# Performance work log

Hardware: AMD Instinct MI355X
Metric: run time of the kernel (lower is better)

## Reference

```python
import jax, jax.numpy as jnp
import numpy as np

N = 4096          # number of video frames (n)
M = 1024          # input feature size (m)
D = 1024          # output_size; must equal M for the grid_sample offset math
APPERTURE = 256   # band half-width: logits with |i-j| >= APPERTURE are masked
SCALE = 0.06      # Q scaling from the original module


def _grid_sample_bilinear(img, gx, gy):
    """F.grid_sample(img[None,None], grid, mode='bilinear', align_corners=True).
    img: (H, W); gx, gy: (H, W) normalized coords in [-1, 1].
    gx indexes the W (last) axis, gy the H axis, matching torch's grid layout."""
    H, W = img.shape
    ix = (gx + 1.0) * (W - 1) * 0.5
    iy = (gy + 1.0) * (H - 1) * 0.5
    ix0 = jnp.floor(ix)
    iy0 = jnp.floor(iy)
    wx = ix - ix0  # weight for the +1 neighbor along W
    wy = iy - iy0  # weight for the +1 neighbor along H
    ix0i = jnp.clip(ix0.astype(jnp.int32), 0, W - 1)
    ix1i = jnp.clip(ix0i + 1, 0, W - 1)
    iy0i = jnp.clip(iy0.astype(jnp.int32), 0, H - 1)
    iy1i = jnp.clip(iy0i + 1, 0, H - 1)
    v00 = img[iy0i, ix0i]
    v01 = img[iy0i, ix1i]
    v10 = img[iy1i, ix0i]
    v11 = img[iy1i, ix1i]
    return (1.0 - wy) * ((1.0 - wx) * v00 + wx * v01) + wy * ((1.0 - wx) * v10 + wx * v11)


def setup_inputs() -> dict:
    key = jax.random.key(0)
    ks = jax.random.split(key, 8)
    s = 0.02
    f32 = jnp.float32
    return {
        "x": jax.random.normal(ks[0], (N, M), f32),
        "Wq": s * jax.random.normal(ks[1], (M, D), f32),
        "Wk": s * jax.random.normal(ks[2], (M, D), f32),
        "Wv": s * jax.random.normal(ks[3], (M, D), f32),
        "Wofx": s * jax.random.normal(ks[4], (D, D), f32),
        "bofx": jnp.zeros((D,), f32),
        "Wofy": s * jax.random.normal(ks[5], (D, D), f32),
        "bofy": jnp.zeros((D,), f32),
        "Wout": s * jax.random.normal(ks[6], (D, M), f32),
    }


def reference(x, Wq, Wk, Wv, Wofx, bofx, Wofy, bofy, Wout):
    H, W = x.shape  # H = n frames, W = m features
    Q = x @ Wq                       # (n, D)
    # offsets are computed from the UNscaled Q (scaling happens later in torch)
    ofx = Q @ Wofx + bofx            # (n, D) == (H, W) since D == W
    ofy = Q @ Wofy + bofy
    # base grid: channel 0 = 2*i/H - 1 (row), channel 1 = 2*j/W - 1 (col);
    # grid_sample reads channel 0 as the x (W-axis) coordinate, channel 1 as y.
    rows = jnp.arange(H, dtype=x.dtype)[:, None]
    cols = jnp.arange(W, dtype=x.dtype)[None, :]
    gx = jnp.clip(2.0 * rows / H - 1.0 + ofx, -1.0, 1.0)  # (H, W)
    gy = jnp.clip(2.0 * cols / W - 1.0 + ofy, -1.0, 1.0)  # (H, W)
    x_new = _grid_sample_bilinear(x, gx, gy)              # (H, W)
    K = x_new @ Wk                   # (n, D)
    V = x_new @ Wv                   # (n, D)
    logits = (SCALE * Q) @ K.T       # (n, n)
    idx = jnp.arange(H)
    band_mask = jnp.abs(idx[:, None] - idx[None, :]) >= APPERTURE
    logits = jnp.where(band_mask, -jnp.inf, logits)
    att = jax.nn.softmax(logits, axis=-1)  # (n, n); dropout is identity at eval
    # torch: y = (V.T @ att).T  ==  att.T @ V  (note the transpose of att!)
    y = att.T @ V                    # (n, D)
    y = y @ Wout                     # (n, m)
    return y, att
```

## Files before the change

kernel.cpp:

```cpp
#include <hip/hip_runtime.h>
#include <hip/hip_bf16.h>
#include <math.h>

#define NN 4096
#define MM 1024
#define BANDP 512

typedef float f4v __attribute__((ext_vector_type(4)));
typedef float f32x4 __attribute__((ext_vector_type(4)));
typedef short bf16x8 __attribute__((ext_vector_type(8)));
typedef short s4v __attribute__((ext_vector_type(4)));
typedef unsigned int u4v __attribute__((ext_vector_type(4)));

__device__ __forceinline__ short f2b(float f) {
    union { float f; unsigned u; } v; v.f = f;
    unsigned r = v.u + 0x7fffu + ((v.u >> 16) & 1u);
    return (short)(r >> 16);
}
__device__ __forceinline__ float b2f(short s) {
    union { unsigned u; float f; } v;
    v.u = ((unsigned)(unsigned short)s) << 16;
    return v.f;
}
__device__ __forceinline__ float b2f_lo(unsigned p) {
    union { unsigned u; float f; } v; v.u = p << 16; return v.f;
}
__device__ __forceinline__ float b2f_hi(unsigned p) {
    union { unsigned u; float f; } v; v.u = p & 0xffff0000u; return v.f;
}

__device__ __forceinline__ void gl2lds16(const void* g, void* l) {
    __builtin_amdgcn_global_load_lds(
        (const __attribute__((address_space(1))) void*)g,
        (__attribute__((address_space(3))) void*)l, 16, 0, 0);
}

#define WAIT_VM8() asm volatile("s_waitcnt vmcnt(8)" ::: "memory")
#define WAIT_VM4() asm volatile("s_waitcnt vmcnt(4)" ::: "memory")
#define WAIT_VM0() asm volatile("s_waitcnt vmcnt(0)" ::: "memory")

__global__ __launch_bounds__(256)
void split_x_k(const float* __restrict__ s, short* __restrict__ h,
               short* __restrict__ l)
{
    const int i = (blockIdx.x * 256 + threadIdx.x) << 2;
    f4v v = *(const f4v*)&s[i];
    s4v hv, lv;
    #pragma unroll
    for (int q = 0; q < 4; ++q) {
        hv[q] = f2b(v[q]);
        lv[q] = f2b(v[q] - b2f(hv[q]));
    }
    *(s4v*)&h[i] = hv;
    *(s4v*)&l[i] = lv;
}

__global__ __launch_bounds__(256)
void build_pairs_k(const float* __restrict__ x, unsigned* __restrict__ pairs)
{
    const int i = blockIdx.x;
    const int t = threadIdx.x;
    const int j4 = t << 2;
    const float* row = x + (size_t)i * MM;
    f4v v = *(const f4v*)&row[j4];
    const float nb = (j4 + 4 < MM) ? row[j4 + 4] : row[MM - 1];
    u4v o;
    #pragma unroll
    for (int q = 0; q < 4; ++q) {
        const float a = v[q];
        const float b = (q < 3) ? v[q + 1] : ((j4 + 4 < MM) ? nb : a);
        o[q] = (unsigned)(unsigned short)f2b(a)
             | ((unsigned)(unsigned short)f2b(b) << 16);
    }
    *(u4v*)&pairs[(size_t)i * MM + j4] = o;
}

__global__ __launch_bounds__(256)
void trsplit_k(const float* __restrict__ W, short* __restrict__ Th,
               short* __restrict__ Tl)
{
    __shared__ float tile[32][33];
    const int bx = blockIdx.x << 5, by = blockIdx.y << 5;
    const int tx = threadIdx.x, ty = threadIdx.y;
    #pragma unroll
    for (int r = ty; r < 32; r += 8)
        tile[r][tx] = W[(size_t)(by + r) * MM + bx + tx];
    __syncthreads();
    #pragma unroll
    for (int r = ty; r < 32; r += 8) {
        const float v = tile[tx][r];
        const short h = f2b(v);
        Th[(size_t)(bx + r) * MM + by + tx] = h;
        Tl[(size_t)(bx + r) * MM + by + tx] = f2b(v - b2f(h));
    }
}

__global__ __launch_bounds__(256)
void transpose_f32_bf16(const float* __restrict__ W, short* __restrict__ Wt)
{
    __shared__ float tile[32][33];
    const int bx = blockIdx.x << 5, by = blockIdx.y << 5;
    const int tx = threadIdx.x, ty = threadIdx.y;
    #pragma unroll
    for (int r = ty; r < 32; r += 8)
        tile[r][tx] = W[(size_t)(by + r) * MM + bx + tx];
    __syncthreads();
    #pragma unroll
    for (int r = ty; r < 32; r += 8)
        Wt[(size_t)(bx + r) * MM + by + tx] = f2b(tile[tx][r]);
}

template<bool BIAS>
__global__ __launch_bounds__(256, 2)
void gemm_split(const short* __restrict__ Ah, const short* __restrict__ Al,
                const short* __restrict__ Bth, const short* __restrict__ Btl,
                const float* __restrict__ bias0, const float* __restrict__ bias1,
                short* __restrict__ outH, short* __restrict__ outL, int N)
{
    __shared__ short As[2][2][128 * 32];
    __shared__ short Bs[2][2][128 * 32];

    const int t  = threadIdx.x;
    const int l  = t & 63;
    const int w  = t >> 6;
    const int wm = w >> 1, wn = w & 1;
    const int lr = l & 15;
    const int lk = (l >> 4) << 3;
    const int lks = lk ^ (((l >> 1) & 3) << 3);

    const int i0 = blockIdx.y << 7;
    const int bn = blockIdx.x << 7;

    const int sr = t >> 2;
    const int sk = (((t & 3) ^ ((t >> 3) & 3)) << 3);

    const short* aH = Ah  + (size_t)(i0 + sr) * MM + sk;
    const short* aL = Al  + (size_t)(i0 + sr) * MM + sk;
    const short* bH = Bth + (size_t)(bn + sr) * MM + sk;
    const short* bL = Btl + (size_t)(bn + sr) * MM + sk;

    f32x4 acc[4][4] = {};

    auto stage = [&](int sb, int k0) {
        gl2lds16(aH + k0,           &As[sb][0][t * 8]);
        gl2lds16(aH + 64 * MM + k0, &As[sb][0][2048 + t * 8]);
        gl2lds16(aL + k0,           &As[sb][1][t * 8]);
        gl2lds16(aL + 64 * MM + k0, &As[sb][1][2048 + t * 8]);
        gl2lds16(bH + k0,           &Bs[sb][0][t * 8]);
        gl2lds16(bH + 64 * MM + k0, &Bs[sb][0][2048 + t * 8]);
        gl2lds16(bL + k0,           &Bs[sb][1][t * 8]);
        gl2lds16(bL + 64 * MM + k0, &Bs[sb][1][2048 + t * 8]);
    };
    stage(0, 0);

    for (int kt = 0; kt < 32; ++kt) {
        const int cur = kt & 1;
        if (kt + 1 < 32) { stage(cur ^ 1, (kt + 1) << 5); WAIT_VM8(); }
        else             { WAIT_VM0(); }
        __builtin_amdgcn_s_barrier();
        __builtin_amdgcn_sched_barrier(0);

        bf16x8 ah[4], al[4], bh[4], bl[4];
        #pragma unroll
        for (int i = 0; i < 4; ++i) {
            ah[i] = *(const bf16x8*)&As[cur][0][(wm * 64 + i * 16 + lr) * 32 + lks];
            al[i] = *(const bf16x8*)&As[cur][1][(wm * 64 + i * 16 + lr) * 32 + lks];
        }
        #pragma unroll
        for (int j = 0; j < 4; ++j) {
            bh[j] = *(const bf16x8*)&Bs[cur][0][(wn * 64 + j * 16 + lr) * 32 + lks];
            bl[j] = *(const bf16x8*)&Bs[cur][1][(wn * 64 + j * 16 + lr) * 32 + lks];
        }
        __builtin_amdgcn_s_setprio(1);
        #pragma unroll
        for (int i = 0; i < 4; ++i)
            #pragma unroll
            for (int j = 0; j < 4; ++j) {
                acc[i][j] = __builtin_amdgcn_mfma_f32_16x16x32_bf16(ah[i], bl[j], acc[i][j], 0, 0, 0);
                acc[i][j] = __builtin_amdgcn_mfma_f32_16x16x32_bf16(al[i], bh[j], acc[i][j], 0, 0, 0);
                acc[i][j] = __builtin_amdgcn_mfma_f32_16x16x32_bf16(ah[i], bh[j], acc[i][j], 0, 0, 0);
            }
        __builtin_amdgcn_s_setprio(0);
        __builtin_amdgcn_s_barrier();
    }

    const int rb = (l >> 4) << 2;
    #pragma unroll
    for (int i = 0; i < 4; ++i)
        #pragma unroll
        for (int j = 0; j < 4; ++j) {
            const int n = bn + wn * 64 + j * 16 + lr;
            float bv = 0.f;
            if (BIAS) bv = (n < 1024) ? bias0[n] : bias1[n - 1024];
            #pragma unroll
            for (int r = 0; r < 4; ++r) {
                const int m = i0 + wm * 64 + i * 16 + rb + r;
                const float v = acc[i][j][r] + bv;
                const short h = f2b(v);
                outH[(size_t)m * N + n] = h;
                outL[(size_t)m * N + n] = f2b(v - b2f(h));
            }
        }
}

__global__ __launch_bounds__(256)
void grid_sample_k(const unsigned* __restrict__ pairs, const short* __restrict__ ofh,
                   const short* __restrict__ ofl, short* __restrict__ xnb)
{
    const int i = blockIdx.x;
    const int tid = threadIdx.x;
    const int j4 = tid << 2;

    const short* rh = ofh + (size_t)i * 2048;
    const short* rl = ofl + (size_t)i * 2048;
    s4v hx = *(const s4v*)&rh[j4];
    s4v lx = *(const s4v*)&rl[j4];
    s4v hy = *(const s4v*)&rh[1024 + j4];
    s4v ly = *(const s4v*)&rl[1024 + j4];
    s4v out;

    const float gxb = (2.0f * (float)i) / (float)NN - 1.0f;

    #pragma unroll
    for (int q = 0; q < 4; ++q) {
        const int j = j4 + q;
        float gx = gxb + b2f(hx[q]) + b2f(lx[q]);
        gx = fminf(fmaxf(gx, -1.0f), 1.0f);
        float gy = (2.0f * (float)j) / (float)MM - 1.0f + b2f(hy[q]) + b2f(ly[q]);
        gy = fminf(fmaxf(gy, -1.0f), 1.0f);

        const float ixf = (gx + 1.0f) * 511.5f;
        const float iyf = (gy + 1.0f) * 2047.5f;
        const float ix0 = floorf(ixf);
        const float iy0 = floorf(iyf);
        const float wx = ixf - ix0;
        const float wy = iyf - iy0;
        int ix0i = (int)ix0; ix0i = max(0, min(ix0i, MM - 1));
        int iy0i = (int)iy0; iy0i = max(0, min(iy0i, NN - 1));
        const int iy1i = min(iy0i + 1, NN - 1);

        const unsigned p0 = pairs[(size_t)iy0i * MM + ix0i];
        const unsigned p1 = pairs[(size_t)iy1i * MM + ix0i];
        const float v00 = b2f_lo(p0), v01 = b2f_hi(p0);
        const float v10 = b2f_lo(p1), v11 = b2f_hi(p1);
        out[q] = f2b((1.0f - wy) * ((1.0f - wx) * v00 + wx * v01)
                   + wy * ((1.0f - wx) * v10 + wx * v11));
    }
    *(s4v*)&xnb[(size_t)i * MM + j4] = out;
}

template<int MODE>
__global__ __launch_bounds__(256, 2)
void mfma_gemm(const short* __restrict__ A, const short* __restrict__ Bt,
               void* __restrict__ C0, void* __restrict__ C1)
{
    __shared__ short As[2][128 * 32];
    __shared__ short Bs[2][128 * 32];

    const int t  = threadIdx.x;
    const int l  = t & 63;
    const int w  = t >> 6;
    const int wm = w >> 1, wn = w & 1;
    const int lr = l & 15;
    const int lk = (l >> 4) << 3;
    const int lks = lk ^ (((l >> 1) & 3) << 3);

    const int i0 = blockIdx.y << 7;
    const int bn = blockIdx.x << 7;
    const int jb = (MODE == 3) ? (i0 - 256 + bn) : bn;

    const int sr = t >> 2;
    const int sk = (((t & 3) ^ ((t >> 3) & 3)) << 3);

    const short* aS = A + (size_t)(i0 + sr) * MM + sk;
    int br0 = jb + sr, br1 = jb + sr + 64;
    if (MODE == 3) {
        br0 = min(max(br0, 0), NN - 1);
        br1 = min(max(br1, 0), NN - 1);
    }
    const short* bS0 = Bt + (size_t)br0 * MM + sk;
    const short* bS1 = Bt + (size_t)br1 * MM + sk;

    f32x4 acc[4][4] = {};

    auto stage = [&](int sb, int k0) {
        gl2lds16(aS + k0,           &As[sb][0] + t * 8);
        gl2lds16(aS + 64 * MM + k0, &As[sb][0] + 2048 + t * 8);
        gl2lds16(bS0 + k0,          &Bs[sb][0] + t * 8);
        gl2lds16(bS1 + k0,          &Bs[sb][0] + 2048 + t * 8);
    };
    stage(0, 0);

    for (int kt = 0; kt < 32; ++kt) {
        const int cur = kt & 1;
        if (kt + 1 < 32) { stage(cur ^ 1, (kt + 1) << 5); WAIT_VM4(); }
        else             { WAIT_VM0(); }
        __builtin_amdgcn_s_barrier();
        __builtin_amdgcn_sched_barrier(0);

        bf16x8 a[4], b[4];
        #pragma unroll
        for (int i = 0; i < 4; ++i)
            a[i] = *(const bf16x8*)&As[cur][(wm * 64 + i * 16 + lr) * 32 + lks];
        #pragma unroll
        for (int j = 0; j < 4; ++j)
            b[j] = *(const bf16x8*)&Bs[cur][(wn * 64 + j * 16 + lr) * 32 + lks];
        __builtin_amdgcn_s_setprio(1);
        #pragma unroll
        for (int i = 0; i < 4; ++i)
            #pragma unroll
            for (int j = 0; j < 4; ++j)
                acc[i][j] = __builtin_amdgcn_mfma_f32_16x16x32_bf16(a[i], b[j], acc[i][j], 0, 0, 0);
        __builtin_amdgcn_s_setprio(0);
        __builtin_amdgcn_s_barrier();
    }

    const int rb = (l >> 4) << 2;
    #pragma unroll
    for (int i = 0; i < 4; ++i) {
        #pragma unroll
        for (int j = 0; j < 4; ++j) {
            const int nl = wn * 64 + j * 16 + lr;
            if (MODE == 4 && bn + nl >= 1024) {
                const int m0 = i0 + wm * 64 + i * 16 + rb;
                s4v o;
                #pragma unroll
                for (int r = 0; r < 4; ++r) o[r] = f2b(acc[i][j][r]);
                *(s4v*)&((short*)C1)[(size_t)(bn + nl - 1024) * NN + m0] = o;
            } else {
                #pragma unroll
                for (int r = 0; r < 4; ++r) {
                    const int m = i0 + wm * 64 + i * 16 + rb + r;
                    const float v = acc[i][j][r];
                    if (MODE == 4) {
                        ((short*)C0)[(size_t)m * MM + bn + nl] = f2b(v);
                    } else if (MODE == 2) {
                        ((float*)C0)[(size_t)m * MM + bn + nl] = v;
                    } else if (MODE == 3) {
                        const int jj = jb + nl;
                        const int ci = jj - m + 255;
                        if (ci >= 0 && ci <= 510)
                            ((float*)C0)[(size_t)m * BANDP + ci] =
                                (jj >= 0 && jj < NN) ? 0.06f * v : -INFINITY;
                    }
                }
            }
        }
    }
}

__global__ __launch_bounds__(256)
void band_softmax(const float* __restrict__ band, float* __restrict__ att,
                  short* __restrict__ bandT)
{
    const int i = blockIdx.x;
    const int tid = threadIdx.x;
    const float* brow = band + (size_t)i * BANDP;

    float v0 = brow[tid];
    float v1 = (tid < 255) ? brow[tid + 256] : -INFINITY;

    float m = fmaxf(v0, v1);
    #pragma unroll
    for (int o = 32; o >= 1; o >>= 1) m = fmaxf(m, __shfl_xor(m, o));
    __shared__ float redm[4], reds[4];
    const int wv = tid >> 6, ln = tid & 63;
    if (ln == 0) redm[wv] = m;
    __syncthreads();
    m = fmaxf(fmaxf(redm[0], redm[1]), fmaxf(redm[2], redm[3]));

    float p0 = expf(v0 - m);
    float p1 = (tid < 255) ? expf(v1 - m) : 0.f;
    float s = p0 + p1;
    #pragma unroll
    for (int o = 32; o >= 1; o >>= 1) s += __shfl_xor(s, o);
    if (ln == 0) reds[wv] = s;
    __syncthreads();
    s = reds[0] + reds[1] + reds[2] + reds[3];
    const float rinv = 1.0f / s;
    p0 *= rinv; p1 *= rinv;

    float* arow = att + (size_t)i * NN;
    f4v z = {0.f, 0.f, 0.f, 0.f};
    #pragma unroll
    for (int q = 0; q < 4; ++q)
        *(f4v*)&arow[(q * 256 + tid) << 2] = z;
    __syncthreads();
    int j = i + tid - 255;
    if (j >= 0 && j < NN) {
        arow[j] = p0;
        bandT[(size_t)j * 768 + (i - (j & ~7) + 384)] = f2b(p0);
    }
    j = i + tid + 1;
    if (tid < 255 && j >= 0 && j < NN) {
        arow[j] = p1;
        bandT[(size_t)j * 768 + (i - (j & ~7) + 384)] = f2b(p1);
    }
}

__global__ __launch_bounds__(256, 2)
void attT_v_mfma(const short* __restrict__ bandT, const short* __restrict__ Vt,
                 short* __restrict__ y1b)
{
    const int t = threadIdx.x, l = t & 63, w = t >> 6;
    const int wm = w >> 1, wn = w & 1;
    const int lr = l & 15, lk = (l >> 4) << 3;
    const int r0 = blockIdx.y << 7;
    const int n0 = blockIdx.x << 6;

    f32x4 acc[4][2] = {};
    for (int ks = 0; ks < 20; ++ks) {
        const int j0 = r0 - 256 + (ks << 5);
        if (j0 < 0 || j0 >= NN) continue;
        bf16x8 b[2];
        #pragma unroll
        for (int j = 0; j < 2; ++j)
            b[j] = *(const bf16x8*)&Vt[(size_t)(n0 + wn * 32 + j * 16 + lr) * NN + j0 + lk];
        #pragma unroll
        for (int i = 0; i < 4; ++i) {
            const int r = r0 + wm * 64 + i * 16 + lr;
            const int cc = j0 + lk - (r & ~7) + 384;
            bf16x8 a = *(const bf16x8*)&bandT[(size_t)r * 768 + cc];
            #pragma unroll
            for (int j = 0; j < 2; ++j)
                acc[i][j] = __builtin_amdgcn_mfma_f32_16x16x32_bf16(a, b[j], acc[i][j], 0, 0, 0);
        }
    }
    const int rb = (l >> 4) << 2;
    #pragma unroll
    for (int i = 0; i < 4; ++i)
        #pragma unroll
        for (int j = 0; j < 2; ++j)
            #pragma unroll
            for (int r = 0; r < 4; ++r)
                y1b[(size_t)(r0 + wm * 64 + i * 16 + rb + r) * MM + n0 + wn * 32 + j * 16 + lr]
                    = f2b(acc[i][j][r]);
}

extern "C" void kernel_launch(void* const* d_in, const int* in_sizes, int n_in,
                              void* d_out, int out_size, void* d_ws, size_t ws_size,
                              hipStream_t stream)
{
    const float* x    = (const float*)d_in[0];
    const float* Wq   = (const float*)d_in[1];
    const float* Wk   = (const float*)d_in[2];
    const float* Wv   = (const float*)d_in[3];
    const float* Wofx = (const float*)d_in[4];
    const float* bofx = (const float*)d_in[5];
    const float* Wofy = (const float*)d_in[6];
    const float* bofy = (const float*)d_in[7];
    const float* Wout = (const float*)d_in[8];

    float* y_out   = (float*)d_out;
    float* att_out = (float*)d_out + (size_t)NN * MM;

    char* wsb = (char*)d_ws;
    const size_t MB = 1024 * 1024;
    short*    Qh      = (short*)(wsb + 0);
    short*    Ql      = (short*)(wsb + 8 * MB);
    short*    xh      = (short*)(wsb + 16 * MB);
    short*    xl      = (short*)(wsb + 24 * MB);
    short*    WqTh    = (short*)(wsb + 32 * MB);
    short*    WqTl    = (short*)(wsb + 34 * MB);
    short*    WofxyTh = (short*)(wsb + 16 * MB);
    short*    WofxyTl = (short*)(wsb + 20 * MB);
    short*    ofxyh   = (short*)(wsb + 32 * MB);
    short*    ofxyl   = (short*)(wsb + 48 * MB);
    unsigned* pairs   = (unsigned*)(wsb + 16 * MB);
    short*    xnb     = (short*)(wsb + 8 * MB);
    short*    WkvT    = (short*)(wsb + 16 * MB);
    short*    WoutT   = (short*)(wsb + 20 * MB);
    short*    Kb      = (short*)(wsb + 24 * MB);
    short*    Vtb     = (short*)(wsb + 32 * MB);
    float*    band    = (float*)(wsb + 40 * MB);
    short*    bandT   = (short*)(wsb + 48 * MB);
    short*    y1b     = (short*)(wsb + 8 * MB);

    const dim3 blk(256);
    const dim3 tgrid(32, 32), tblk(32, 8);

    split_x_k<<<dim3(4096), blk, 0, stream>>>(x, xh, xl);
    trsplit_k<<<tgrid, tblk, 0, stream>>>(Wq, WqTh, WqTl);
    gemm_split<false><<<dim3(8, 32), blk, 0, stream>>>(
        xh, xl, WqTh, WqTl, nullptr, nullptr, Qh, Ql, 1024);
    trsplit_k<<<tgrid, tblk, 0, stream>>>(Wofx, WofxyTh, WofxyTl);
    trsplit_k<<<tgrid, tblk, 0, stream>>>(Wofy, WofxyTh + 1024 * 1024, WofxyTl + 1024 * 1024);
    gemm_split<true><<<dim3(16, 32), blk, 0, stream>>>(
        Qh, Ql, WofxyTh, WofxyTl, bofx, bofy, ofxyh, ofxyl, 2048);

    build_pairs_k<<<dim3(NN), blk, 0, stream>>>(x, pairs);
    grid_sample_k<<<dim3(NN), blk, 0, stream>>>(pairs, ofxyh, ofxyl, xnb);

    transpose_f32_bf16<<<tgrid, tblk, 0, stream>>>(Wk, WkvT);
    transpose_f32_bf16<<<tgrid, tblk, 0, stream>>>(Wv, WkvT + 1024 * 1024);
    transpose_f32_bf16<<<tgrid, tblk, 0, stream>>>(Wout, WoutT);

    mfma_gemm<4><<<dim3(16, 32), blk, 0, stream>>>(xnb, WkvT, Kb, Vtb);
    mfma_gemm<3><<<dim3(5, 32), blk, 0, stream>>>(Qh, Kb, band, nullptr);
    hipMemsetAsync(bandT, 0, (size_t)NN * 768 * sizeof(short), stream);
    band_softmax<<<dim3(NN), blk, 0, stream>>>(band, att_out, bandT);
    attT_v_mfma<<<dim3(16, 32), blk, 0, stream>>>(bandT, Vtb, y1b);
    mfma_gemm<2><<<dim3(8, 32), blk, 0, stream>>>(y1b, WoutT, y_out, nullptr);
}
```

Baseline: 348.1 us.

## Sample from transposed bf16 copy of x for coalesced grid-sample gathers

```diff
diff --git a/kernel.cpp b/kernel.cpp
--- a/kernel.cpp
+++ b/kernel.cpp
@@ -10,7 +10,6 @@
 typedef float f32x4 __attribute__((ext_vector_type(4)));
 typedef short bf16x8 __attribute__((ext_vector_type(8)));
 typedef short s4v __attribute__((ext_vector_type(4)));
-typedef unsigned int u4v __attribute__((ext_vector_type(4)));
 
 __device__ __forceinline__ short f2b(float f) {
     union { float f; unsigned u; } v; v.f = f;
@@ -22,12 +21,6 @@
     v.u = ((unsigned)(unsigned short)s) << 16;
     return v.f;
 }
-__device__ __forceinline__ float b2f_lo(unsigned p) {
-    union { unsigned u; float f; } v; v.u = p << 16; return v.f;
-}
-__device__ __forceinline__ float b2f_hi(unsigned p) {
-    union { unsigned u; float f; } v; v.u = p & 0xffff0000u; return v.f;
-}
 
 __device__ __forceinline__ void gl2lds16(const void* g, void* l) {
     __builtin_amdgcn_global_load_lds(
@@ -56,23 +49,19 @@
 }
 
 __global__ __launch_bounds__(256)
-void build_pairs_k(const float* __restrict__ x, unsigned* __restrict__ pairs)
-{
-    const int i = blockIdx.x;
-    const int t = threadIdx.x;
-    const int j4 = t << 2;
-    const float* row = x + (size_t)i * MM;
-    f4v v = *(const f4v*)&row[j4];
-    const float nb = (j4 + 4 < MM) ? row[j4 + 4] : row[MM - 1];
-    u4v o;
-    #pragma unroll
-    for (int q = 0; q < 4; ++q) {
-        const float a = v[q];
-        const float b = (q < 3) ? v[q + 1] : ((j4 + 4 < MM) ? nb : a);
-        o[q] = (unsigned)(unsigned short)f2b(a)
-             | ((unsigned)(unsigned short)f2b(b) << 16);
-    }
-    *(u4v*)&pairs[(size_t)i * MM + j4] = o;
+void transpose_x_k(const float* __restrict__ x, short* __restrict__ xT)
+{
+    __shared__ float tile[32][33];
+    const int bx = blockIdx.x << 5;
+    const int by = blockIdx.y << 5;
+    const int tx = threadIdx.x, ty = threadIdx.y;
+    #pragma unroll
+    for (int r = ty; r < 32; r += 8)
+        tile[r][tx] = x[(size_t)(by + r) * MM + bx + tx];
+    __syncthreads();
+    #pragma unroll
+    for (int r = ty; r < 32; r += 8)
+        xT[(size_t)(bx + r) * NN + by + tx] = f2b(tile[tx][r]);
 }
 
 __global__ __launch_bounds__(256)
@@ -204,10 +193,11 @@
 }
 
 __global__ __launch_bounds__(256)
-void grid_sample_k(const unsigned* __restrict__ pairs, const short* __restrict__ ofh,
+void grid_sample_k(const short* __restrict__ xT, const short* __restrict__ ofh,
                    const short* __restrict__ ofl, short* __restrict__ xnb)
 {
-    const int i = blockIdx.x;
+    const int bid = blockIdx.x;
+    const int i = ((bid & 7) << 9) | (bid >> 3);
     const int tid = threadIdx.x;
     const int j4 = tid << 2;
 
@@ -237,12 +227,13 @@
         const float wy = iyf - iy0;
         int ix0i = (int)ix0; ix0i = max(0, min(ix0i, MM - 1));
         int iy0i = (int)iy0; iy0i = max(0, min(iy0i, NN - 1));
+        const int ix1i = min(ix0i + 1, MM - 1);
         const int iy1i = min(iy0i + 1, NN - 1);
 
-        const unsigned p0 = pairs[(size_t)iy0i * MM + ix0i];
-        const unsigned p1 = pairs[(size_t)iy1i * MM + ix0i];
-        const float v00 = b2f_lo(p0), v01 = b2f_hi(p0);
-        const float v10 = b2f_lo(p1), v11 = b2f_hi(p1);
+        const short* c0 = xT + (size_t)ix0i * NN;
+        const short* c1 = xT + (size_t)ix1i * NN;
+        const float v00 = b2f(c0[iy0i]), v01 = b2f(c1[iy0i]);
+        const float v10 = b2f(c0[iy1i]), v11 = b2f(c1[iy1i]);
         out[q] = f2b((1.0f - wy) * ((1.0f - wx) * v00 + wx * v01)
                    + wy * ((1.0f - wx) * v10 + wx * v11));
     }
@@ -458,6 +449,7 @@
     const size_t MB = 1024 * 1024;
     short*    Qh      = (short*)(wsb + 0);
     short*    Ql      = (short*)(wsb + 8 * MB);
+    short*    xT      = (short*)(wsb + 8 * MB);
     short*    xh      = (short*)(wsb + 16 * MB);
     short*    xl      = (short*)(wsb + 24 * MB);
     short*    WqTh    = (short*)(wsb + 32 * MB);
@@ -466,15 +458,14 @@
     short*    WofxyTl = (short*)(wsb + 20 * MB);
     short*    ofxyh   = (short*)(wsb + 32 * MB);
     short*    ofxyl   = (short*)(wsb + 48 * MB);
-    unsigned* pairs   = (unsigned*)(wsb + 16 * MB);
-    short*    xnb     = (short*)(wsb + 8 * MB);
-    short*    WkvT    = (short*)(wsb + 16 * MB);
-    short*    WoutT   = (short*)(wsb + 20 * MB);
+    short*    xnb     = (short*)(wsb + 16 * MB);
+    short*    WkvT    = (short*)(wsb + 8 * MB);
+    short*    WoutT   = (short*)(wsb + 12 * MB);
     short*    Kb      = (short*)(wsb + 24 * MB);
     short*    Vtb     = (short*)(wsb + 32 * MB);
     float*    band    = (float*)(wsb + 40 * MB);
     short*    bandT   = (short*)(wsb + 48 * MB);
-    short*    y1b     = (short*)(wsb + 8 * MB);
+    short*    y1b     = (short*)(wsb + 16 * MB);
 
     const dim3 blk(256);
     const dim3 tgrid(32, 32), tblk(32, 8);
@@ -488,8 +479,8 @@
     gemm_split<true><<<dim3(16, 32), blk, 0, stream>>>(
         Qh, Ql, WofxyTh, WofxyTl, bofx, bofy, ofxyh, ofxyl, 2048);
 
-    build_pairs_k<<<dim3(NN), blk, 0, stream>>>(x, pairs);
-    grid_sample_k<<<dim3(NN), blk, 0, stream>>>(pairs, ofxyh, ofxyl, xnb);
+    transpose_x_k<<<dim3(32, 128), tblk, 0, stream>>>(x, xT);
+    grid_sample_k<<<dim3(NN), blk, 0, stream>>>(xT, ofxyh, ofxyl, xnb);
 
     transpose_f32_bf16<<<tgrid, tblk, 0, stream>>>(Wk, WkvT);
     transpose_f32_bf16<<<tgrid, tblk, 0, stream>>>(Wv, WkvT + 1024 * 1024);
```

Result: slower. 358.9 us (+3.1%).
